# Kernel tuning notes

Measured on AMD Instinct MI355X. Metric: run time of the kernel, lower is better.

## Reference

```python
import jax, jax.numpy as jnp
import numpy as np

C = 256
HEADS = 8
HD = C // HEADS
EPS = 1e-5


def _layernorm(x, g, b):
    mu = jnp.mean(x, axis=-1, keepdims=True)
    var = jnp.var(x, axis=-1, keepdims=True)
    return (x - mu) * jax.lax.rsqrt(var + EPS) * g + b


def setup_inputs() -> dict:
    key = jax.random.key(0)
    ks = jax.random.split(key, 16)
    s = 0.02
    return {
        "x": jax.random.normal(ks[0], (1, C, 64, 64), jnp.float32),
        "bn_gamma": 1.0 + s * jax.random.normal(ks[1], (C,), jnp.float32),
        "bn_beta": s * jax.random.normal(ks[2], (C,), jnp.float32),
        "bn_mean": s * jax.random.normal(ks[3], (C,), jnp.float32),
        "bn_var": jnp.ones((C,), jnp.float32),
        "w_in": s * jax.random.normal(ks[4], (C, C), jnp.float32),
        "b_in": jnp.zeros((C,), jnp.float32),
        "ln1_g": jnp.ones((C,), jnp.float32),
        "ln1_b": jnp.zeros((C,), jnp.float32),
        "w_qkv": s * jax.random.normal(ks[5], (3 * C, C), jnp.float32),
        "b_qkv": jnp.zeros((3 * C,), jnp.float32),
        "w_ap": s * jax.random.normal(ks[6], (C, C), jnp.float32),
        "b_ap": jnp.zeros((C,), jnp.float32),
        "ln2_g": jnp.ones((C,), jnp.float32),
        "ln2_b": jnp.zeros((C,), jnp.float32),
        "w_ff1": s * jax.random.normal(ks[7], (4 * C, C), jnp.float32),
        "b_ff1": jnp.zeros((4 * C,), jnp.float32),
        "w_ff2": s * jax.random.normal(ks[8], (C, 4 * C), jnp.float32),
        "b_ff2": jnp.zeros((C,), jnp.float32),
        "w_out": s * jax.random.normal(ks[9], (C, C), jnp.float32),
        "b_out": jnp.zeros((C,), jnp.float32),
    }


def reference(x, bn_gamma, bn_beta, bn_mean, bn_var, w_in, b_in,
              ln1_g, ln1_b, w_qkv, b_qkv, w_ap, b_ap,
              ln2_g, ln2_b, w_ff1, b_ff1, w_ff2, b_ff2, w_out, b_out):
    b, c, h, w = x.shape
    t = h * w
    x_in = x
    # BatchNorm2d (eval mode: running stats)
    xn = (x - bn_mean[None, :, None, None]) * jax.lax.rsqrt(bn_var + EPS)[None, :, None, None]
    xn = xn * bn_gamma[None, :, None, None] + bn_beta[None, :, None, None]
    # proj_in 1x1 conv -> tokens [b, t, c]
    tok = xn.reshape(b, c, t).transpose(0, 2, 1)
    tok = tok @ w_in.T + b_in
    # transformer block (depth=1)
    y = _layernorm(tok, ln1_g, ln1_b)  # norm1
    qkv = y @ w_qkv.T + b_qkv  # [b, t, 3c], channel split (3, H, hd)
    qkv = qkv.reshape(b, t, 3, HEADS, HD)
    q = qkv[:, :, 0].transpose(0, 2, 1, 3)  # [b, H, t, hd]
    k = qkv[:, :, 1].transpose(0, 2, 1, 3)
    v = qkv[:, :, 2].transpose(0, 2, 1, 3)
    scale = HD ** (-0.5)
    attn = jax.nn.softmax(jnp.einsum('bhqd,bhkd->bhqk', q, k) * scale, axis=-1)
    o = jnp.einsum('bhqk,bhkd->bhqd', attn, v)  # [b, H, t, hd]
    o = o.transpose(0, 2, 1, 3).reshape(b, t, c)  # channels ordered (H, hd)
    o = o @ w_ap.T + b_ap  # attn proj 1x1
    attn_out = o + y  # VanillaAttention residual adds its (normed) input
    tok = tok + attn_out
    # FFN
    z = _layernorm(tok, ln2_g, ln2_b)
    z = jax.nn.gelu(z @ w_ff1.T + b_ff1, approximate=False)
    tok = tok + (z @ w_ff2.T + b_ff2)
    # back to image, proj_out 1x1, outer residual
    x4 = tok.transpose(0, 2, 1).reshape(b, c, h, w)
    out = jnp.einsum('oc,bchw->bohw', w_out, x4) + b_out[None, :, None, None]
    return out + x_in
```

## Files before the change

kernel.cpp:

```cpp
#include <hip/hip_runtime.h>
#include <math.h>

#define T_TOK 4096
#define C_DIM 256
#define EPSF  1e-5f
#define SC_QL (0.17677669529663687f * 1.4426950408889634f)

typedef short  bf16x8  __attribute__((ext_vector_type(8)));
typedef float  f32x4   __attribute__((ext_vector_type(4)));
typedef ushort ushort8 __attribute__((ext_vector_type(8)));

__device__ __forceinline__ short f2bf(float f) {
    unsigned u = __builtin_bit_cast(unsigned, f);
    unsigned r = (u + 0x7FFFu + ((u >> 16) & 1u)) >> 16;
    return (short)r;
}
__device__ __forceinline__ float bf2f(ushort u) {
    return __builtin_bit_cast(float, ((unsigned)u) << 16);
}
__device__ __forceinline__ unsigned pk_bf16(float a, float b) {
    const unsigned ua = __builtin_bit_cast(unsigned, a) + 0x8000u;
    const unsigned ub = __builtin_bit_cast(unsigned, b) + 0x8000u;
    return __builtin_amdgcn_perm(ub, ua, 0x07060302u);
}
template <int CTRL>
__device__ __forceinline__ float dppf(float x) {
    return __builtin_bit_cast(float,
        __builtin_amdgcn_mov_dpp(__builtin_bit_cast(int, x), CTRL, 0xF, 0xF, true));
}
__device__ __forceinline__ float rowsum16(float x) {
    x += dppf<0xB1>(x);
    x += dppf<0x4E>(x);
    x += dppf<0x141>(x);
    x += dppf<0x140>(x);
    return x;
}
#define MFMA16(a, b, c) __builtin_amdgcn_mfma_f32_16x16x32_bf16(a, b, c, 0, 0, 0)

__global__ __launch_bounds__(256) void prep_kernel(
    const float* __restrict__ w_in, const float* __restrict__ w_qkv,
    const float* __restrict__ w_ap, const float* __restrict__ w_ff1,
    const float* __restrict__ w_ff2, const float* __restrict__ w_out,
    const float* __restrict__ b_qkv, ushort* __restrict__ wbuf,
    float* __restrict__ bqs,
    const float* __restrict__ x, const float* __restrict__ gamma,
    const float* __restrict__ beta, const float* __restrict__ mean,
    const float* __restrict__ var, ushort* __restrict__ tin)
{
    __shared__ float tile[32][33];
    if (blockIdx.x < 896) {
        const int gid = blockIdx.x * 256 + threadIdx.x;
        const int e0 = gid * 4;
        const float* src; int off; float sc = 1.f;
        if (e0 < 65536)       { src = w_in;  off = e0; }
        else if (e0 < 262144) { src = w_qkv; off = e0 - 65536; if (off < 65536) sc = SC_QL; }
        else if (e0 < 327680) { src = w_ap;  off = e0 - 262144; }
        else if (e0 < 589824) { src = w_ff1; off = e0 - 327680; }
        else if (e0 < 851968) { src = w_ff2; off = e0 - 589824; }
        else                  { src = w_out; off = e0 - 851968; }
        const float4 v = *(const float4*)(src + off);
        ushort4 o;
        o.x = (ushort)f2bf(v.x * sc); o.y = (ushort)f2bf(v.y * sc);
        o.z = (ushort)f2bf(v.z * sc); o.w = (ushort)f2bf(v.w * sc);
        *(ushort4*)(wbuf + e0) = o;
        if (gid < 192) {
            const float s2 = (gid < 64) ? SC_QL : 1.f;
            float4 b = ((const float4*)b_qkv)[gid];
            b.x *= s2; b.y *= s2; b.z *= s2; b.w *= s2;
            ((float4*)bqs)[gid] = b;
        }
    } else {
        const int bidx = blockIdx.x - 896;
        const int t0 = (bidx & 127) * 32, c0 = (bidx >> 7) * 32;
        const int tx = threadIdx.x & 31, ty = threadIdx.x >> 5;
#pragma unroll
        for (int i = 0; i < 32; i += 8) {
            const int c = c0 + ty + i;
            const float a = rsqrtf(var[c] + EPSF) * gamma[c];
            const float d = beta[c] - mean[c] * a;
            tile[ty + i][tx] = x[c * T_TOK + t0 + tx] * a + d;
        }
        __syncthreads();
#pragma unroll
        for (int i = 0; i < 32; i += 8) {
            const int t = t0 + ty + i;
            tin[t * C_DIM + c0 + tx] = (ushort)f2bf(tile[tx][ty + i]);
        }
    }
}

__global__ __launch_bounds__(256) void fused_pre(
    const ushort* __restrict__ tin, const ushort* __restrict__ wb_in,
    const float* __restrict__ b_in, const float* __restrict__ ln1_g,
    const float* __restrict__ ln1_b, const ushort* __restrict__ wb_qkv,
    const float* __restrict__ bqs, float* __restrict__ tok0,
    float* __restrict__ yout, ushort* __restrict__ qkvb)
{
    __shared__ ushort Atile[16 * 264];
    __shared__ ushort Ytile[16 * 264];
    __shared__ float  red[4][16][2];
    const int t0 = blockIdx.x * 16;
    const int tid = threadIdx.x, wv = tid >> 6, lane = tid & 63;
    const int c = lane & 15, g = lane >> 4;

    {
        const int r = tid >> 4, c0 = (tid & 15) * 16;
        const ushort8 a0 = *(const ushort8*)(tin + (size_t)(t0 + r) * 256 + c0);
        const ushort8 a1 = *(const ushort8*)(tin + (size_t)(t0 + r) * 256 + c0 + 8);
        *(ushort8*)&Atile[r * 264 + c0] = a0;
        *(ushort8*)&Atile[r * 264 + c0 + 8] = a1;
    }
    __syncthreads();

    f32x4 accp[4] = {};
#pragma unroll 1
    for (int kc = 0; kc < 8; ++kc) {
        const bf16x8 af = *(const bf16x8*)&Atile[c * 264 + kc * 32 + g * 8];
#pragma unroll
        for (int nf = 0; nf < 4; ++nf) {
            const bf16x8 bfv = *(const bf16x8*)(wb_in +
                (size_t)(wv * 64 + nf * 16 + c) * 256 + kc * 32 + g * 8);
            accp[nf] = MFMA16(af, bfv, accp[nf]);
        }
    }
    float vs[4][4];
    float s1[4] = {}, s2[4] = {};
#pragma unroll
    for (int nf = 0; nf < 4; ++nf) {
        const int col = wv * 64 + nf * 16 + c;
        const float bb = b_in[col];
#pragma unroll
        for (int rr = 0; rr < 4; ++rr) {
            const float v = accp[nf][rr] + bb;
            vs[nf][rr] = v;
            s1[rr] += v;
            s2[rr] += v * v;
            tok0[(size_t)(t0 + 4 * g + rr) * 256 + col] = v;
        }
    }
#pragma unroll
    for (int rr = 0; rr < 4; ++rr) { s1[rr] = rowsum16(s1[rr]); s2[rr] = rowsum16(s2[rr]); }
    if (c == 0) {
#pragma unroll
        for (int rr = 0; rr < 4; ++rr) {
            red[wv][4 * g + rr][0] = s1[rr];
            red[wv][4 * g + rr][1] = s2[rr];
        }
    }
    __syncthreads();
    float mu[4], rs[4];
#pragma unroll
    for (int rr = 0; rr < 4; ++rr) {
        const int row = 4 * g + rr;
        const float S  = red[0][row][0] + red[1][row][0] + red[2][row][0] + red[3][row][0];
        const float S2 = red[0][row][1] + red[1][row][1] + red[2][row][1] + red[3][row][1];
        mu[rr] = S * (1.0f / 256.0f);
        const float var = S2 * (1.0f / 256.0f) - mu[rr] * mu[rr];
        rs[rr] = rsqrtf(var + EPSF);
    }
#pragma unroll
    for (int nf = 0; nf < 4; ++nf) {
        const int col = wv * 64 + nf * 16 + c;
        const float gg = ln1_g[col], bb = ln1_b[col];
#pragma unroll
        for (int rr = 0; rr < 4; ++rr) {
            const float yv = (vs[nf][rr] - mu[rr]) * rs[rr] * gg + bb;
            yout[(size_t)(t0 + 4 * g + rr) * 256 + col] = yv;
            Ytile[(4 * g + rr) * 264 + col] = (ushort)f2bf(yv);
        }
    }
    __syncthreads();

    f32x4 accq[12] = {};
#pragma unroll 1
    for (int kc = 0; kc < 8; ++kc) {
        const bf16x8 af = *(const bf16x8*)&Ytile[c * 264 + kc * 32 + g * 8];
#pragma unroll
        for (int nf = 0; nf < 12; ++nf) {
            const bf16x8 bfv = *(const bf16x8*)(wb_qkv +
                (size_t)(wv * 192 + nf * 16 + c) * 256 + kc * 32 + g * 8);
            accq[nf] = MFMA16(af, bfv, accq[nf]);
        }
    }
#pragma unroll
    for (int nf = 0; nf < 12; ++nf) {
        const int col = wv * 192 + nf * 16 + c;
        const float bb = bqs[col];
#pragma unroll
        for (int rr = 0; rr < 4; ++rr)
            qkvb[(size_t)(t0 + 4 * g + rr) * 768 + col] = (ushort)f2bf(accq[nf][rr] + bb);
    }
}

#define KS   40
#define VTS  72
#define PS_W 36

__global__ __launch_bounds__(256) void attn_mfma(
    const ushort* __restrict__ qkv, ushort* __restrict__ o1,
    ushort* __restrict__ o2, float* __restrict__ lpart)
{
    const int h    = blockIdx.y;
    const int q0   = blockIdx.x << 6;
    const int half = blockIdx.z;
    const int tid  = threadIdx.x;
    const int wv   = tid >> 6, lane = tid & 63;
    const int c    = lane & 15, g = lane >> 4;

    __shared__ ushort Ks[2][64 * KS];
    __shared__ ushort Vt[2][32 * VTS];
    __shared__ float  Ps[4][16 * PS_W];

    const bf16x8 qf = *(const bf16x8*)(qkv + (size_t)(q0 + wv * 16 + c) * 768 + h * 32 + g * 8);

    bf16x8 ones;
#pragma unroll
    for (int i = 0; i < 8; ++i) ones[i] = (short)0x3F80;

    f32x4 oacc0 = {0.f, 0.f, 0.f, 0.f};
    f32x4 oacc1 = {0.f, 0.f, 0.f, 0.f};
    f32x4 oaccl = {0.f, 0.f, 0.f, 0.f};

    const int kr = tid >> 2, kc = (tid & 3) * 8;
    const int vp = tid & 31, vd = (tid >> 5) * 4;
    const ushort* kbase = qkv + 256 + h * 32;
    const ushort* vbase = qkv + 512 + h * 32;

    const int kt0 = half * 32, kt1 = kt0 + 32;
    ushort8 kpre  = *(const ushort8*)(kbase + ((size_t)kt0 * 64 + kr) * 768 + kc);
    ushort4 vpre0 = *(const ushort4*)(vbase + ((size_t)kt0 * 64 + 2 * vp) * 768 + vd);
    ushort4 vpre1 = *(const ushort4*)(vbase + ((size_t)kt0 * 64 + 2 * vp + 1) * 768 + vd);

    int p = 0;
    for (int kt = kt0; kt < kt1; ++kt) {
        *(ushort8*)&Ks[p][kr * KS + kc] = kpre;
        {
            unsigned* vtp = (unsigned*)&Vt[p][0];
            vtp[(vd + 0) * (VTS / 2) + vp] = (unsigned)vpre0.x | ((unsigned)vpre1.x << 16);
            vtp[(vd + 1) * (VTS / 2) + vp] = (unsigned)vpre0.y | ((unsigned)vpre1.y << 16);
            vtp[(vd + 2) * (VTS / 2) + vp] = (unsigned)vpre0.z | ((unsigned)vpre1.z << 16);
            vtp[(vd + 3) * (VTS / 2) + vp] = (unsigned)vpre0.w | ((unsigned)vpre1.w << 16);
        }
        __syncthreads();
        if (kt + 1 < kt1) {
            const size_t t0 = (size_t)(kt + 1) * 64;
            kpre  = *(const ushort8*)(kbase + (t0 + kr) * 768 + kc);
            vpre0 = *(const ushort4*)(vbase + (t0 + 2 * vp) * 768 + vd);
            vpre1 = *(const ushort4*)(vbase + (t0 + 2 * vp + 1) * 768 + vd);
        }

        const ushort* ks = &Ks[p][0];
        const ushort* vt = &Vt[p][0];
        const f32x4 zz = {0.f, 0.f, 0.f, 0.f};
        const bf16x8 k0 = *(const bf16x8*)&ks[(0 * 16 + c) * KS + g * 8];
        const bf16x8 k1 = *(const bf16x8*)&ks[(1 * 16 + c) * KS + g * 8];
        const bf16x8 k2 = *(const bf16x8*)&ks[(2 * 16 + c) * KS + g * 8];
        const bf16x8 k3 = *(const bf16x8*)&ks[(3 * 16 + c) * KS + g * 8];
        const f32x4 s0 = MFMA16(k0, qf, zz);
        const f32x4 s1 = MFMA16(k1, qf, zz);
        const f32x4 s2 = MFMA16(k2, qf, zz);
        const f32x4 s3 = MFMA16(k3, qf, zz);

        float* prow = &Ps[wv][c * PS_W];
        {
            const float e00 = __builtin_amdgcn_exp2f(s0[0]), e01 = __builtin_amdgcn_exp2f(s0[1]);
            const float e02 = __builtin_amdgcn_exp2f(s0[2]), e03 = __builtin_amdgcn_exp2f(s0[3]);
            const float e10 = __builtin_amdgcn_exp2f(s1[0]), e11 = __builtin_amdgcn_exp2f(s1[1]);
            const float e12 = __builtin_amdgcn_exp2f(s1[2]), e13 = __builtin_amdgcn_exp2f(s1[3]);
            const float e20 = __builtin_amdgcn_exp2f(s2[0]), e21 = __builtin_amdgcn_exp2f(s2[1]);
            const float e22 = __builtin_amdgcn_exp2f(s2[2]), e23 = __builtin_amdgcn_exp2f(s2[3]);
            const float e30 = __builtin_amdgcn_exp2f(s3[0]), e31 = __builtin_amdgcn_exp2f(s3[1]);
            const float e32 = __builtin_amdgcn_exp2f(s3[2]), e33 = __builtin_amdgcn_exp2f(s3[3]);
            prow[0 * 8 + 2 * g + 0] = __builtin_bit_cast(float, pk_bf16(e00, e01));
            prow[0 * 8 + 2 * g + 1] = __builtin_bit_cast(float, pk_bf16(e02, e03));
            prow[1 * 8 + 2 * g + 0] = __builtin_bit_cast(float, pk_bf16(e10, e11));
            prow[1 * 8 + 2 * g + 1] = __builtin_bit_cast(float, pk_bf16(e12, e13));
            prow[2 * 8 + 2 * g + 0] = __builtin_bit_cast(float, pk_bf16(e20, e21));
            prow[2 * 8 + 2 * g + 1] = __builtin_bit_cast(float, pk_bf16(e22, e23));
            prow[3 * 8 + 2 * g + 0] = __builtin_bit_cast(float, pk_bf16(e30, e31));
            prow[3 * 8 + 2 * g + 1] = __builtin_bit_cast(float, pk_bf16(e32, e33));
        }
#pragma unroll
        for (int ch = 0; ch < 2; ++ch) {
            const bf16x8 pf = *(const bf16x8*)&prow[ch * 16 + 4 * g];
            const bf16x8 v0 = *(const bf16x8*)&vt[(c)      * VTS + ch * 32 + g * 8];
            const bf16x8 v1 = *(const bf16x8*)&vt[(16 + c) * VTS + ch * 32 + g * 8];
            oacc0 = MFMA16(pf, v0, oacc0);
            oacc1 = MFMA16(pf, v1, oacc1);
            oaccl = MFMA16(pf, ones, oaccl);
        }
        p ^= 1;
        __syncthreads();
    }

    {
        ushort* op = (half ? o2 : o1) + (size_t)(q0 + wv * 16) * 256 + h * 32;
#pragma unroll
        for (int rr = 0; rr < 4; ++rr) {
            op[(4 * g + rr) * 256 + c]      = (ushort)f2bf(oacc0[rr]);
            op[(4 * g + rr) * 256 + 16 + c] = (ushort)f2bf(oacc1[rr]);
        }
        if (c == 0) {
#pragma unroll
            for (int rr = 0; rr < 4; ++rr)
                lpart[(size_t)(q0 + wv * 16 + 4 * g + rr) * 16 + half * 8 + h] = oaccl[rr];
        }
    }
}

__global__ __launch_bounds__(256) void fused_mid(
    const ushort* __restrict__ o1, const ushort* __restrict__ o2,
    const float* __restrict__ lpart, const ushort* __restrict__ wb_ap,
    const float* __restrict__ b_ap, const float* __restrict__ yin,
    const float* __restrict__ tok0, const float* __restrict__ ln2_g,
    const float* __restrict__ ln2_b, const ushort* __restrict__ wb_ff1,
    const float* __restrict__ b_ff1, float* __restrict__ tok1,
    ushort* __restrict__ zbuf)
{
    __shared__ ushort Otile[16 * 264];
    __shared__ ushort Ztile[16 * 264];
    __shared__ float  red[4][16][2];
    const int t0 = blockIdx.x * 16;
    const int tid = threadIdx.x, wv = tid >> 6, lane = tid & 63;
    const int c = lane & 15, g = lane >> 4;

    {
        const int r = tid >> 4, c0 = (tid & 15) * 16;
        const int h = (tid & 15) >> 1;
        const float inv = 1.0f / (lpart[(size_t)(t0 + r) * 16 + h] +
                                  lpart[(size_t)(t0 + r) * 16 + 8 + h]);
        const ushort8 a0 = *(const ushort8*)(o1 + (size_t)(t0 + r) * 256 + c0);
        const ushort8 a1 = *(const ushort8*)(o1 + (size_t)(t0 + r) * 256 + c0 + 8);
        const ushort8 b0 = *(const ushort8*)(o2 + (size_t)(t0 + r) * 256 + c0);
        const ushort8 b1 = *(const ushort8*)(o2 + (size_t)(t0 + r) * 256 + c0 + 8);
        unsigned w[4];
#pragma unroll
        for (int i = 0; i < 4; ++i) {
            const float v0 = (bf2f(a0[2 * i]) + bf2f(b0[2 * i])) * inv;
            const float v1 = (bf2f(a0[2 * i + 1]) + bf2f(b0[2 * i + 1])) * inv;
            w[i] = pk_bf16(v0, v1);
        }
        *(ushort8*)&Otile[r * 264 + c0] = *(ushort8*)w;
#pragma unroll
        for (int i = 0; i < 4; ++i) {
            const float v0 = (bf2f(a1[2 * i]) + bf2f(b1[2 * i])) * inv;
            const float v1 = (bf2f(a1[2 * i + 1]) + bf2f(b1[2 * i + 1])) * inv;
            w[i] = pk_bf16(v0, v1);
        }
        *(ushort8*)&Otile[r * 264 + c0 + 8] = *(ushort8*)w;
    }
    __syncthreads();

    f32x4 accp[4] = {};
#pragma unroll 1
    for (int kc = 0; kc < 8; ++kc) {
        const bf16x8 af = *(const bf16x8*)&Otile[c * 264 + kc * 32 + g * 8];
#pragma unroll
        for (int nf = 0; nf < 4; ++nf) {
            const bf16x8 bfv = *(const bf16x8*)(wb_ap +
                (size_t)(wv * 64 + nf * 16 + c) * 256 + kc * 32 + g * 8);
            accp[nf] = MFMA16(af, bfv, accp[nf]);
        }
    }
    float vs[4][4];
    float s1[4] = {}, s2[4] = {};
#pragma unroll
    for (int nf = 0; nf < 4; ++nf) {
        const int col = wv * 64 + nf * 16 + c;
        const float bb = b_ap[col];
#pragma unroll
        for (int rr = 0; rr < 4; ++rr) {
            const size_t idx = (size_t)(t0 + 4 * g + rr) * 256 + col;
            const float v = accp[nf][rr] + bb + yin[idx] + tok0[idx];
            vs[nf][rr] = v;
            s1[rr] += v;
            s2[rr] += v * v;
            tok1[idx] = v;
        }
    }
#pragma unroll
    for (int rr = 0; rr < 4; ++rr) { s1[rr] = rowsum16(s1[rr]); s2[rr] = rowsum16(s2[rr]); }
    if (c == 0) {
#pragma unroll
        for (int rr = 0; rr < 4; ++rr) {
            red[wv][4 * g + rr][0] = s1[rr];
            red[wv][4 * g + rr][1] = s2[rr];
        }
    }
    __syncthreads();
    float mu[4], rs[4];
#pragma unroll
    for (int rr = 0; rr < 4; ++rr) {
        const int row = 4 * g + rr;
        const float S  = red[0][row][0] + red[1][row][0] + red[2][row][0] + red[3][row][0];
        const float S2 = red[0][row][1] + red[1][row][1] + red[2][row][1] + red[3][row][1];
        mu[rr] = S * (1.0f / 256.0f);
        const float var = S2 * (1.0f / 256.0f) - mu[rr] * mu[rr];
        rs[rr] = rsqrtf(var + EPSF);
    }
#pragma unroll
    for (int nf = 0; nf < 4; ++nf) {
        const int col = wv * 64 + nf * 16 + c;
        const float gg = ln2_g[col], bb = ln2_b[col];
#pragma unroll
        for (int rr = 0; rr < 4; ++rr) {
            const float zv = (vs[nf][rr] - mu[rr]) * rs[rr] * gg + bb;
            Ztile[(4 * g + rr) * 264 + col] = (ushort)f2bf(zv);
        }
    }
    __syncthreads();

    f32x4 accf[16] = {};
#pragma unroll 1
    for (int kc = 0; kc < 8; ++kc) {
        const bf16x8 af = *(const bf16x8*)&Ztile[c * 264 + kc * 32 + g * 8];
#pragma unroll
        for (int nf = 0; nf < 16; ++nf) {
            const bf16x8 bfv = *(const bf16x8*)(wb_ff1 +
                (size_t)(wv * 256 + nf * 16 + c) * 256 + kc * 32 + g * 8);
            accf[nf] = MFMA16(af, bfv, accf[nf]);
        }
    }
#pragma unroll
    for (int nf = 0; nf < 16; ++nf) {
        const int col = wv * 256 + nf * 16 + c;
        const float bb = b_ff1[col];
#pragma unroll
        for (int rr = 0; rr < 4; ++rr) {
            float v = accf[nf][rr] + bb;
            v = 0.5f * v * (1.0f + erff(v * 0.70710678118654752f));
            zbuf[(size_t)(t0 + 4 * g + rr) * 1024 + col] = (ushort)f2bf(v);
        }
    }
}

__global__ __launch_bounds__(256) void fused_post(
    const ushort* __restrict__ zbuf, const ushort* __restrict__ wb_ff2,
    const float* __restrict__ b_ff2, const float* __restrict__ tok1,
    const ushort* __restrict__ wb_out, const float* __restrict__ b_out,
    const float* __restrict__ x, float* __restrict__ out)
{
    __shared__ ushort Ztile[16 * 1032];
    __shared__ ushort T2tile[16 * 264];
    const int t0 = blockIdx.x * 16;
    const int tid = threadIdx.x, wv = tid >> 6, lane = tid & 63;
    const int c = lane & 15, g = lane >> 4;

    {
        const int r = tid >> 4, c0 = (tid & 15) * 64;
#pragma unroll
        for (int i = 0; i < 8; ++i) {
            const ushort8 zv = *(const ushort8*)(zbuf + (size_t)(t0 + r) * 1024 + c0 + i * 8);
            *(ushort8*)&Ztile[r * 1032 + c0 + i * 8] = zv;
        }
    }
    __syncthreads();

    f32x4 accf[4] = {};
#pragma unroll 1
    for (int kc = 0; kc < 32; ++kc) {
        const bf16x8 af = *(const bf16x8*)&Ztile[c * 1032 + kc * 32 + g * 8];
#pragma unroll
        for (int nf = 0; nf < 4; ++nf) {
            const bf16x8 bfv = *(const bf16x8*)(wb_ff2 +
                (size_t)(wv * 64 + nf * 16 + c) * 1024 + kc * 32 + g * 8);
            accf[nf] = MFMA16(af, bfv, accf[nf]);
        }
    }
#pragma unroll
    for (int nf = 0; nf < 4; ++nf) {
        const int col = wv * 64 + nf * 16 + c;
        const float bb = b_ff2[col];
#pragma unroll
        for (int rr = 0; rr < 4; ++rr) {
            const size_t idx = (size_t)(t0 + 4 * g + rr) * 256 + col;
            const float v = accf[nf][rr] + bb + tok1[idx];
            T2tile[(4 * g + rr) * 264 + col] = (ushort)f2bf(v);
        }
    }
    __syncthreads();

    f32x4 acco[4] = {};
#pragma unroll 1
    for (int kc = 0; kc < 8; ++kc) {
        const bf16x8 bfr = *(const bf16x8*)&T2tile[c * 264 + kc * 32 + g * 8];
#pragma unroll
        for (int mf = 0; mf < 4; ++mf) {
            const bf16x8 afr = *(const bf16x8*)(wb_out +
                (size_t)(wv * 64 + mf * 16 + c) * 256 + kc * 32 + g * 8);
            acco[mf] = MFMA16(afr, bfr, acco[mf]);
        }
    }
#pragma unroll
    for (int mf = 0; mf < 4; ++mf) {
#pragma unroll
        for (int rr = 0; rr < 4; ++rr) {
            const int och = wv * 64 + mf * 16 + 4 * g + rr;
            const size_t idx = (size_t)och * T_TOK + t0 + c;
            out[idx] = acco[mf][rr] + b_out[och] + x[idx];
        }
    }
}

extern "C" void kernel_launch(void* const* d_in, const int* in_sizes, int n_in,
                              void* d_out, int out_size, void* d_ws, size_t ws_size,
                              hipStream_t stream)
{
    const float* x     = (const float*)d_in[0];
    const float* bn_g  = (const float*)d_in[1];
    const float* bn_b  = (const float*)d_in[2];
    const float* bn_m  = (const float*)d_in[3];
    const float* bn_v  = (const float*)d_in[4];
    const float* w_in  = (const float*)d_in[5];
    const float* b_in  = (const float*)d_in[6];
    const float* ln1_g = (const float*)d_in[7];
    const float* ln1_b = (const float*)d_in[8];
    const float* w_qkv = (const float*)d_in[9];
    const float* b_qkv = (const float*)d_in[10];
    const float* w_ap  = (const float*)d_in[11];
    const float* b_ap  = (const float*)d_in[12];
    const float* ln2_g = (const float*)d_in[13];
    const float* ln2_b = (const float*)d_in[14];
    const float* w_ff1 = (const float*)d_in[15];
    const float* b_ff1 = (const float*)d_in[16];
    const float* w_ff2 = (const float*)d_in[17];
    const float* b_ff2 = (const float*)d_in[18];
    const float* w_out = (const float*)d_in[19];
    const float* b_out = (const float*)d_in[20];
    float* out = (float*)d_out;
    float* ws  = (float*)d_ws;

    const size_t MF = 1u << 20;
    float*  tok0   = ws;
    float*  y      = ws + MF;
    float*  tok1   = ws + 2 * MF;
    ushort* qkv_bf = (ushort*)(ws + 3 * MF);
    ushort* zbuf   = (ushort*)(ws + 4 * MF + MF / 2);
    ushort* tin_bf = (ushort*)(ws + 6 * MF + MF / 2);
    ushort* o1p    = tin_bf;
    ushort* o2p    = (ushort*)(ws + 7 * MF);
    float*  lpart  = ws + 7 * MF + MF / 2;
    ushort* wbuf   = (ushort*)(ws + 7 * MF + MF / 2 + 65536);
    const ushort* wb_in  = wbuf;
    const ushort* wb_qkv = wbuf + 65536;
    const ushort* wb_ap  = wbuf + 262144;
    const ushort* wb_ff1 = wbuf + 327680;
    const ushort* wb_ff2 = wbuf + 589824;
    const ushort* wb_out = wbuf + 851968;
    float* bqs = (float*)(wbuf + 917504);

    prep_kernel<<<1920, 256, 0, stream>>>(w_in, w_qkv, w_ap, w_ff1, w_ff2, w_out,
                                          b_qkv, wbuf, bqs,
                                          x, bn_g, bn_b, bn_m, bn_v, tin_bf);
    fused_pre<<<256, 256, 0, stream>>>(tin_bf, wb_in, b_in, ln1_g, ln1_b,
                                       wb_qkv, bqs, tok0, y, qkv_bf);
    attn_mfma<<<dim3(64, 8, 2), 256, 0, stream>>>(qkv_bf, o1p, o2p, lpart);
    fused_mid<<<256, 256, 0, stream>>>(o1p, o2p, lpart, wb_ap, b_ap, y, tok0,
                                       ln2_g, ln2_b, wb_ff1, b_ff1, tok1, zbuf);
    fused_post<<<256, 256, 0, stream>>>(zbuf, wb_ff2, b_ff2, tok1, wb_out, b_out,
                                        x, out);
}
```

Baseline: 213.9 us.

## Widen fused token kernels to 1024 threads with one column fragment per wave

The three fused per-token kernels (pre, mid, post) go from 256 to 1024 threads per block, so 16 waves each own a 16-column slice instead of 4 waves owning 64 columns. The LayerNorm row reductions now combine partial sums across 16 waves through shared memory with an extra reduction step and barrier. The goal is more in-flight waves to hide the latency of streaming the weight matrices from global memory, since only 256 blocks launch. In exchange there are extra synchronisation barriers, per-wave register and unroll pressure, and each block repeats the shared A-tile reads across more waves.

```diff
diff --git a/kernel.cpp b/kernel.cpp
--- a/kernel.cpp
+++ b/kernel.cpp
@@ -89,7 +89,7 @@
     }
 }
 
-__global__ __launch_bounds__(256) void fused_pre(
+__global__ __launch_bounds__(1024) void fused_pre(
     const ushort* __restrict__ tin, const ushort* __restrict__ wb_in,
     const float* __restrict__ b_in, const float* __restrict__ ln1_g,
     const float* __restrict__ ln1_b, const ushort* __restrict__ wb_qkv,
@@ -98,93 +98,81 @@
 {
     __shared__ ushort Atile[16 * 264];
     __shared__ ushort Ytile[16 * 264];
-    __shared__ float  red[4][16][2];
+    __shared__ float  red[16][16][2];
     const int t0 = blockIdx.x * 16;
     const int tid = threadIdx.x, wv = tid >> 6, lane = tid & 63;
     const int c = lane & 15, g = lane >> 4;
 
     {
-        const int r = tid >> 4, c0 = (tid & 15) * 16;
-        const ushort8 a0 = *(const ushort8*)(tin + (size_t)(t0 + r) * 256 + c0);
-        const ushort8 a1 = *(const ushort8*)(tin + (size_t)(t0 + r) * 256 + c0 + 8);
-        *(ushort8*)&Atile[r * 264 + c0] = a0;
-        *(ushort8*)&Atile[r * 264 + c0 + 8] = a1;
+        const int r = tid >> 6, c0 = (tid & 63) * 4;
+        *(ushort4*)&Atile[r * 264 + c0] = *(const ushort4*)(tin + (size_t)(t0 + r) * 256 + c0);
     }
     __syncthreads();
 
-    f32x4 accp[4] = {};
-#pragma unroll 1
+    f32x4 accp = {};
+#pragma unroll
     for (int kc = 0; kc < 8; ++kc) {
         const bf16x8 af = *(const bf16x8*)&Atile[c * 264 + kc * 32 + g * 8];
-#pragma unroll
-        for (int nf = 0; nf < 4; ++nf) {
-            const bf16x8 bfv = *(const bf16x8*)(wb_in +
-                (size_t)(wv * 64 + nf * 16 + c) * 256 + kc * 32 + g * 8);
-            accp[nf] = MFMA16(af, bfv, accp[nf]);
-        }
-    }
-    float vs[4][4];
-    float s1[4] = {}, s2[4] = {};
-#pragma unroll
-    for (int nf = 0; nf < 4; ++nf) {
-        const int col = wv * 64 + nf * 16 + c;
-        const float bb = b_in[col];
-#pragma unroll
-        for (int rr = 0; rr < 4; ++rr) {
-            const float v = accp[nf][rr] + bb;
-            vs[nf][rr] = v;
-            s1[rr] += v;
-            s2[rr] += v * v;
-            tok0[(size_t)(t0 + 4 * g + rr) * 256 + col] = v;
-        }
-    }
-#pragma unroll
-    for (int rr = 0; rr < 4; ++rr) { s1[rr] = rowsum16(s1[rr]); s2[rr] = rowsum16(s2[rr]); }
-    if (c == 0) {
-#pragma unroll
-        for (int rr = 0; rr < 4; ++rr) {
-            red[wv][4 * g + rr][0] = s1[rr];
-            red[wv][4 * g + rr][1] = s2[rr];
+        const bf16x8 bfv = *(const bf16x8*)(wb_in +
+            (size_t)(wv * 16 + c) * 256 + kc * 32 + g * 8);
+        accp = MFMA16(af, bfv, accp);
+    }
+    const int colp = wv * 16 + c;
+    {
+        const float bb = b_in[colp];
+        float vs[4], s1[4], s2[4];
+#pragma unroll
+        for (int rr = 0; rr < 4; ++rr) {
+            const float v = accp[rr] + bb;
+            vs[rr] = v; s1[rr] = v; s2[rr] = v * v;
+            tok0[(size_t)(t0 + 4 * g + rr) * 256 + colp] = v;
+        }
+#pragma unroll
+        for (int rr = 0; rr < 4; ++rr) { s1[rr] = rowsum16(s1[rr]); s2[rr] = rowsum16(s2[rr]); }
+        if (c == 0) {
+#pragma unroll
+            for (int rr = 0; rr < 4; ++rr) {
+                red[wv][4 * g + rr][0] = s1[rr];
+                red[wv][4 * g + rr][1] = s2[rr];
+            }
+        }
+        __syncthreads();
+        if (tid < 32) {
+            const int row = tid >> 1, j = tid & 1;
+            float s = 0.f;
+#pragma unroll
+            for (int w = 0; w < 16; ++w) s += red[w][row][j];
+            red[0][row][j] = s;
+        }
+        __syncthreads();
+        const float gg = ln1_g[colp], lb = ln1_b[colp];
+#pragma unroll
+        for (int rr = 0; rr < 4; ++rr) {
+            const int row = 4 * g + rr;
+            const float mu = red[0][row][0] * (1.0f / 256.0f);
+            const float var = red[0][row][1] * (1.0f / 256.0f) - mu * mu;
+            const float rs = rsqrtf(var + EPSF);
+            const float yv = (vs[rr] - mu) * rs * gg + lb;
+            yout[(size_t)(t0 + row) * 256 + colp] = yv;
+            Ytile[row * 264 + colp] = (ushort)f2bf(yv);
         }
     }
     __syncthreads();
-    float mu[4], rs[4];
-#pragma unroll
-    for (int rr = 0; rr < 4; ++rr) {
-        const int row = 4 * g + rr;
-        const float S  = red[0][row][0] + red[1][row][0] + red[2][row][0] + red[3][row][0];
-        const float S2 = red[0][row][1] + red[1][row][1] + red[2][row][1] + red[3][row][1];
-        mu[rr] = S * (1.0f / 256.0f);
-        const float var = S2 * (1.0f / 256.0f) - mu[rr] * mu[rr];
-        rs[rr] = rsqrtf(var + EPSF);
-    }
-#pragma unroll
-    for (int nf = 0; nf < 4; ++nf) {
-        const int col = wv * 64 + nf * 16 + c;
-        const float gg = ln1_g[col], bb = ln1_b[col];
-#pragma unroll
-        for (int rr = 0; rr < 4; ++rr) {
-            const float yv = (vs[nf][rr] - mu[rr]) * rs[rr] * gg + bb;
-            yout[(size_t)(t0 + 4 * g + rr) * 256 + col] = yv;
-            Ytile[(4 * g + rr) * 264 + col] = (ushort)f2bf(yv);
-        }
-    }
-    __syncthreads();
-
-    f32x4 accq[12] = {};
-#pragma unroll 1
+
+    f32x4 accq[3] = {};
+#pragma unroll
     for (int kc = 0; kc < 8; ++kc) {
         const bf16x8 af = *(const bf16x8*)&Ytile[c * 264 + kc * 32 + g * 8];
 #pragma unroll
-        for (int nf = 0; nf < 12; ++nf) {
+        for (int nf = 0; nf < 3; ++nf) {
             const bf16x8 bfv = *(const bf16x8*)(wb_qkv +
-                (size_t)(wv * 192 + nf * 16 + c) * 256 + kc * 32 + g * 8);
+                (size_t)(wv * 48 + nf * 16 + c) * 256 + kc * 32 + g * 8);
             accq[nf] = MFMA16(af, bfv, accq[nf]);
         }
     }
 #pragma unroll
-    for (int nf = 0; nf < 12; ++nf) {
-        const int col = wv * 192 + nf * 16 + c;
+    for (int nf = 0; nf < 3; ++nf) {
+        const int col = wv * 48 + nf * 16 + c;
         const float bb = bqs[col];
 #pragma unroll
         for (int rr = 0; rr < 4; ++rr)
@@ -308,7 +296,7 @@
     }
 }
 
-__global__ __launch_bounds__(256) void fused_mid(
+__global__ __launch_bounds__(1024) void fused_mid(
     const ushort* __restrict__ o1, const ushort* __restrict__ o2,
     const float* __restrict__ lpart, const ushort* __restrict__ wb_ap,
     const float* __restrict__ b_ap, const float* __restrict__ yin,
@@ -319,111 +307,89 @@
 {
     __shared__ ushort Otile[16 * 264];
     __shared__ ushort Ztile[16 * 264];
-    __shared__ float  red[4][16][2];
+    __shared__ float  red[16][16][2];
     const int t0 = blockIdx.x * 16;
     const int tid = threadIdx.x, wv = tid >> 6, lane = tid & 63;
     const int c = lane & 15, g = lane >> 4;
 
     {
-        const int r = tid >> 4, c0 = (tid & 15) * 16;
-        const int h = (tid & 15) >> 1;
+        const int r = tid >> 6, c0 = (tid & 63) * 4;
+        const int h = (tid & 63) >> 3;
         const float inv = 1.0f / (lpart[(size_t)(t0 + r) * 16 + h] +
                                   lpart[(size_t)(t0 + r) * 16 + 8 + h]);
-        const ushort8 a0 = *(const ushort8*)(o1 + (size_t)(t0 + r) * 256 + c0);
-        const ushort8 a1 = *(const ushort8*)(o1 + (size_t)(t0 + r) * 256 + c0 + 8);
-        const ushort8 b0 = *(const ushort8*)(o2 + (size_t)(t0 + r) * 256 + c0);
-        const ushort8 b1 = *(const ushort8*)(o2 + (size_t)(t0 + r) * 256 + c0 + 8);
-        unsigned w[4];
-#pragma unroll
-        for (int i = 0; i < 4; ++i) {
-            const float v0 = (bf2f(a0[2 * i]) + bf2f(b0[2 * i])) * inv;
-            const float v1 = (bf2f(a0[2 * i + 1]) + bf2f(b0[2 * i + 1])) * inv;
-            w[i] = pk_bf16(v0, v1);
-        }
-        *(ushort8*)&Otile[r * 264 + c0] = *(ushort8*)w;
-#pragma unroll
-        for (int i = 0; i < 4; ++i) {
-            const float v0 = (bf2f(a1[2 * i]) + bf2f(b1[2 * i])) * inv;
-            const float v1 = (bf2f(a1[2 * i + 1]) + bf2f(b1[2 * i + 1])) * inv;
-            w[i] = pk_bf16(v0, v1);
-        }
-        *(ushort8*)&Otile[r * 264 + c0 + 8] = *(ushort8*)w;
+        const ushort4 a = *(const ushort4*)(o1 + (size_t)(t0 + r) * 256 + c0);
+        const ushort4 b = *(const ushort4*)(o2 + (size_t)(t0 + r) * 256 + c0);
+        unsigned w[2];
+        w[0] = pk_bf16((bf2f(a.x) + bf2f(b.x)) * inv, (bf2f(a.y) + bf2f(b.y)) * inv);
+        w[1] = pk_bf16((bf2f(a.z) + bf2f(b.z)) * inv, (bf2f(a.w) + bf2f(b.w)) * inv);
+        *(ushort4*)&Otile[r * 264 + c0] = *(ushort4*)w;
     }
     __syncthreads();
 
-    f32x4 accp[4] = {};
-#pragma unroll 1
+    f32x4 accp = {};
+#pragma unroll
     for (int kc = 0; kc < 8; ++kc) {
         const bf16x8 af = *(const bf16x8*)&Otile[c * 264 + kc * 32 + g * 8];
+        const bf16x8 bfv = *(const bf16x8*)(wb_ap +
+            (size_t)(wv * 16 + c) * 256 + kc * 32 + g * 8);
+        accp = MFMA16(af, bfv, accp);
+    }
+    const int colp = wv * 16 + c;
+    {
+        const float bb = b_ap[colp];
+        float vs[4], s1[4], s2[4];
+#pragma unroll
+        for (int rr = 0; rr < 4; ++rr) {
+            const size_t idx = (size_t)(t0 + 4 * g + rr) * 256 + colp;
+            const float v = accp[rr] + bb + yin[idx] + tok0[idx];
+            vs[rr] = v; s1[rr] = v; s2[rr] = v * v;
+            tok1[idx] = v;
+        }
+#pragma unroll
+        for (int rr = 0; rr < 4; ++rr) { s1[rr] = rowsum16(s1[rr]); s2[rr] = rowsum16(s2[rr]); }
+        if (c == 0) {
+#pragma unroll
+            for (int rr = 0; rr < 4; ++rr) {
+                red[wv][4 * g + rr][0] = s1[rr];
+                red[wv][4 * g + rr][1] = s2[rr];
+            }
+        }
+        __syncthreads();
+        if (tid < 32) {
+            const int row = tid >> 1, j = tid & 1;
+            float s = 0.f;
+#pragma unroll
+            for (int w = 0; w < 16; ++w) s += red[w][row][j];
+            red[0][row][j] = s;
+        }
+        __syncthreads();
+        const float gg = ln2_g[colp], lb = ln2_b[colp];
+#pragma unroll
+        for (int rr = 0; rr < 4; ++rr) {
+            const int row = 4 * g + rr;
+            const float mu = red[0][row][0] * (1.0f / 256.0f);
+            const float var = red[0][row][1] * (1.0f / 256.0f) - mu * mu;
+            const float rs = rsqrtf(var + EPSF);
+            const float zv = (vs[rr] - mu) * rs * gg + lb;
+            Ztile[row * 264 + colp] = (ushort)f2bf(zv);
+        }
+    }
+    __syncthreads();
+
+    f32x4 accf[4] = {};
+#pragma unroll
+    for (int kc = 0; kc < 8; ++kc) {
+        const bf16x8 af = *(const bf16x8*)&Ztile[c * 264 + kc * 32 + g * 8];
 #pragma unroll
         for (int nf = 0; nf < 4; ++nf) {
-            const bf16x8 bfv = *(const bf16x8*)(wb_ap +
+            const bf16x8 bfv = *(const bf16x8*)(wb_ff1 +
                 (size_t)(wv * 64 + nf * 16 + c) * 256 + kc * 32 + g * 8);
-            accp[nf] = MFMA16(af, bfv, accp[nf]);
-        }
-    }
-    float vs[4][4];
-    float s1[4] = {}, s2[4] = {};
+            accf[nf] = MFMA16(af, bfv, accf[nf]);
+        }
+    }
 #pragma unroll
     for (int nf = 0; nf < 4; ++nf) {
         const int col = wv * 64 + nf * 16 + c;
-        const float bb = b_ap[col];
-#pragma unroll
-        for (int rr = 0; rr < 4; ++rr) {
-            const size_t idx = (size_t)(t0 + 4 * g + rr) * 256 + col;
-            const float v = accp[nf][rr] + bb + yin[idx] + tok0[idx];
-            vs[nf][rr] = v;
-            s1[rr] += v;
-            s2[rr] += v * v;
-            tok1[idx] = v;
-        }
-    }
-#pragma unroll
-    for (int rr = 0; rr < 4; ++rr) { s1[rr] = rowsum16(s1[rr]); s2[rr] = rowsum16(s2[rr]); }
-    if (c == 0) {
-#pragma unroll
-        for (int rr = 0; rr < 4; ++rr) {
-            red[wv][4 * g + rr][0] = s1[rr];
-            red[wv][4 * g + rr][1] = s2[rr];
-        }
-    }
-    __syncthreads();
-    float mu[4], rs[4];
-#pragma unroll
-    for (int rr = 0; rr < 4; ++rr) {
-        const int row = 4 * g + rr;
-        const float S  = red[0][row][0] + red[1][row][0] + red[2][row][0] + red[3][row][0];
-        const float S2 = red[0][row][1] + red[1][row][1] + red[2][row][1] + red[3][row][1];
-        mu[rr] = S * (1.0f / 256.0f);
-        const float var = S2 * (1.0f / 256.0f) - mu[rr] * mu[rr];
-        rs[rr] = rsqrtf(var + EPSF);
-    }
-#pragma unroll
-    for (int nf = 0; nf < 4; ++nf) {
-        const int col = wv * 64 + nf * 16 + c;
-        const float gg = ln2_g[col], bb = ln2_b[col];
-#pragma unroll
-        for (int rr = 0; rr < 4; ++rr) {
-            const float zv = (vs[nf][rr] - mu[rr]) * rs[rr] * gg + bb;
-            Ztile[(4 * g + rr) * 264 + col] = (ushort)f2bf(zv);
-        }
-    }
-    __syncthreads();
-
-    f32x4 accf[16] = {};
-#pragma unroll 1
-    for (int kc = 0; kc < 8; ++kc) {
-        const bf16x8 af = *(const bf16x8*)&Ztile[c * 264 + kc * 32 + g * 8];
-#pragma unroll
-        for (int nf = 0; nf < 16; ++nf) {
-            const bf16x8 bfv = *(const bf16x8*)(wb_ff1 +
-                (size_t)(wv * 256 + nf * 16 + c) * 256 + kc * 32 + g * 8);
-            accf[nf] = MFMA16(af, bfv, accf[nf]);
-        }
-    }
-#pragma unroll
-    for (int nf = 0; nf < 16; ++nf) {
-        const int col = wv * 256 + nf * 16 + c;
         const float bb = b_ff1[col];
 #pragma unroll
         for (int rr = 0; rr < 4; ++rr) {
@@ -434,7 +400,7 @@
     }
 }
 
-__global__ __launch_bounds__(256) void fused_post(
+__global__ __launch_bounds__(1024) void fused_post(
     const ushort* __restrict__ zbuf, const ushort* __restrict__ wb_ff2,
     const float* __restrict__ b_ff2, const float* __restrict__ tok1,
     const ushort* __restrict__ wb_out, const float* __restrict__ b_out,
@@ -447,58 +413,47 @@
     const int c = lane & 15, g = lane >> 4;
 
     {
-        const int r = tid >> 4, c0 = (tid & 15) * 64;
-#pragma unroll
-        for (int i = 0; i < 8; ++i) {
-            const ushort8 zv = *(const ushort8*)(zbuf + (size_t)(t0 + r) * 1024 + c0 + i * 8);
-            *(ushort8*)&Ztile[r * 1032 + c0 + i * 8] = zv;
-        }
+        const int r = tid >> 6, c0 = (tid & 63) * 16;
+        *(ushort8*)&Ztile[r * 1032 + c0] =
+            *(const ushort8*)(zbuf + (size_t)(t0 + r) * 1024 + c0);
+        *(ushort8*)&Ztile[r * 1032 + c0 + 8] =
+            *(const ushort8*)(zbuf + (size_t)(t0 + r) * 1024 + c0 + 8);
     }
     __syncthreads();
 
-    f32x4 accf[4] = {};
-#pragma unroll 1
+    f32x4 accf = {};
+#pragma unroll
     for (int kc = 0; kc < 32; ++kc) {
         const bf16x8 af = *(const bf16x8*)&Ztile[c * 1032 + kc * 32 + g * 8];
-#pragma unroll
-        for (int nf = 0; nf < 4; ++nf) {
-            const bf16x8 bfv = *(const bf16x8*)(wb_ff2 +
-                (size_t)(wv * 64 + nf * 16 + c) * 1024 + kc * 32 + g * 8);
-            accf[nf] = MFMA16(af, bfv, accf[nf]);
-        }
-    }
-#pragma unroll
-    for (int nf = 0; nf < 4; ++nf) {
-        const int col = wv * 64 + nf * 16 + c;
+        const bf16x8 bfv = *(const bf16x8*)(wb_ff2 +
+            (size_t)(wv * 16 + c) * 1024 + kc * 32 + g * 8);
+        accf = MFMA16(af, bfv, accf);
+    }
+    {
+        const int col = wv * 16 + c;
         const float bb = b_ff2[col];
 #pragma unroll
         for (int rr = 0; rr < 4; ++rr) {
             const size_t idx = (size_t)(t0 + 4 * g + rr) * 256 + col;
-            const float v = accf[nf][rr] + bb + tok1[idx];
+            const float v = accf[rr] + bb + tok1[idx];
             T2tile[(4 * g + rr) * 264 + col] = (ushort)f2bf(v);
         }
     }
     __syncthreads();
 
-    f32x4 acco[4] = {};
-#pragma unroll 1
+    f32x4 acco = {};
+#pragma unroll
     for (int kc = 0; kc < 8; ++kc) {
         const bf16x8 bfr = *(const bf16x8*)&T2tile[c * 264 + kc * 32 + g * 8];
-#pragma unroll
-        for (int mf = 0; mf < 4; ++mf) {
-            const bf16x8 afr = *(const bf16x8*)(wb_out +
-                (size_t)(wv * 64 + mf * 16 + c) * 256 + kc * 32 + g * 8);
-            acco[mf] = MFMA16(afr, bfr, acco[mf]);
-        }
-    }
-#pragma unroll
-    for (int mf = 0; mf < 4; ++mf) {
-#pragma unroll
-        for (int rr = 0; rr < 4; ++rr) {
-            const int och = wv * 64 + mf * 16 + 4 * g + rr;
-            const size_t idx = (size_t)och * T_TOK + t0 + c;
-            out[idx] = acco[mf][rr] + b_out[och] + x[idx];
-        }
+        const bf16x8 afr = *(const bf16x8*)(wb_out +
+            (size_t)(wv * 16 + c) * 256 + kc * 32 + g * 8);
+        acco = MFMA16(afr, bfr, acco);
+    }
+#pragma unroll
+    for (int rr = 0; rr < 4; ++rr) {
+        const int och = wv * 16 + 4 * g + rr;
+        const size_t idx = (size_t)och * T_TOK + t0 + c;
+        out[idx] = acco[rr] + b_out[och] + x[idx];
     }
 }
 
@@ -552,11 +507,11 @@
     prep_kernel<<<1920, 256, 0, stream>>>(w_in, w_qkv, w_ap, w_ff1, w_ff2, w_out,
                                           b_qkv, wbuf, bqs,
                                           x, bn_g, bn_b, bn_m, bn_v, tin_bf);
-    fused_pre<<<256, 256, 0, stream>>>(tin_bf, wb_in, b_in, ln1_g, ln1_b,
-                                       wb_qkv, bqs, tok0, y, qkv_bf);
+    fused_pre<<<256, 1024, 0, stream>>>(tin_bf, wb_in, b_in, ln1_g, ln1_b,
+                                        wb_qkv, bqs, tok0, y, qkv_bf);
     attn_mfma<<<dim3(64, 8, 2), 256, 0, stream>>>(qkv_bf, o1p, o2p, lpart);
-    fused_mid<<<256, 256, 0, stream>>>(o1p, o2p, lpart, wb_ap, b_ap, y, tok0,
-                                       ln2_g, ln2_b, wb_ff1, b_ff1, tok1, zbuf);
-    fused_post<<<256, 256, 0, stream>>>(zbuf, wb_ff2, b_ff2, tok1, wb_out, b_out,
-                                        x, out);
-}
+    fused_mid<<<256, 1024, 0, stream>>>(o1p, o2p, lpart, wb_ap, b_ap, y, tok0,
+                                        ln2_g, ln2_b, wb_ff1, b_ff1, tok1, zbuf);
+    fused_post<<<256, 1024, 0, stream>>>(zbuf, wb_ff2, b_ff2, tok1, wb_out, b_out,
+                                         x, out);
+}
```

After: 204.8 us. 4.3% less time.
